# Performance work log

Hardware: AMD Instinct MI355X
Metric: run time of the kernel (lower is better)

Reference implementation:

```python
import jax, jax.numpy as jnp
import numpy as np


def _get_pairs(top_k_centers):
    """Returns (p0, p1) int32 arrays of shape [B, S]: for each object a, the
    IoU-best partner a', ordered so the larger-L1 box comes first (as in source)."""
    cx, cy, h, w = jnp.split(top_k_centers, 4, axis=-1)  # [B,S,1] each, cxcyhw
    box = jnp.concatenate([cx - 0.5 * w, cy - 0.5 * h, cx + 0.5 * w, cy + 0.5 * h], axis=-1)  # [B,S,4] xyxy
    S = box.shape[1]
    b1 = box[:, :, None, :]  # [B,S,1,4]
    b2 = box[:, None, :, :]  # [B,1,S,4]
    inter_mins = jnp.maximum(b1[..., :2], b2[..., :2])
    inter_maxs = jnp.maximum(b1[..., 2:], b2[..., 2:])  # NOTE: source uses maximum here (kept faithful)
    inter_wh = jnp.clip(inter_maxs - inter_mins, 0.0)
    inter_area = inter_wh[..., 0] * inter_wh[..., 1]  # [B,S,S]
    area = (box[..., 2] - box[..., 0]) * (box[..., 3] - box[..., 1])  # [B,S]
    union = area[:, :, None] + area[:, None, :] - inter_area
    iou = inter_area / union - jnp.eye(S, dtype=inter_area.dtype)
    partner = jnp.argmax(iou, axis=-1)  # [B,S] int
    self_idx = jnp.broadcast_to(jnp.arange(S), partner.shape)
    l1 = jnp.abs(box[..., 2] - box[..., 0]) + jnp.abs(box[..., 3] - box[..., 1])  # [B,S]
    l1_partner = jnp.take_along_axis(l1, partner, axis=-1)
    keep = l1 >= l1_partner  # larger-L1 element goes first
    p0 = jnp.where(keep, self_idx, partner)
    p1 = jnp.where(keep, partner, self_idx)
    return p0, p1


def _gather_pair(a2, p):
    # a2: [B,H,S,S]; p: [B,S]. out[b,h,a,c] = a2[b,h,p[b,a],p[b,c]]
    rows = jnp.take_along_axis(a2, p[:, None, :, None], axis=2)
    return jnp.take_along_axis(rows, p[:, None, None, :], axis=3)


def setup_inputs() -> dict:
    key = jax.random.key(0)
    kq, kk, kv, kc = jax.random.split(key, 4)
    B, H, S, D = 8, 8, 1024, 64
    return {
        "query": jax.random.normal(kq, (B, H, S, D), dtype=jnp.float32),
        "key": jax.random.normal(kk, (B, H, S, D), dtype=jnp.float32),
        "value": jax.random.normal(kv, (B, H, S, D), dtype=jnp.float32),
        "top_k_centers": jax.random.uniform(kc, (B, S, 4), dtype=jnp.float32),
    }


def reference(query, key, value, top_k_centers):
    B, H, S, D = query.shape
    p0, p1 = _get_pairs(top_k_centers)
    # A2(a,b) = <q_{pi_a}, k_{pi_b}> + <q_{pi_a'}, k_{pi_b'}>
    a2 = jnp.einsum('bhqd,bhkd->bhqk', query, key)  # [B,H,S,S]
    scores = (_gather_pair(a2, p0) + _gather_pair(a2, p1)) * (1.0 / np.sqrt(2.0 * D))
    attn = jax.nn.softmax(scores, axis=-1)
    o2 = jnp.einsum('bhqk,bhkd->bhqd', attn, value)  # [B,H,S,D]
    return o2.transpose(0, 2, 1, 3).reshape(B, S, H * D)
```

## Files before the change

### kernel.cpp

```cpp
#include <hip/hip_runtime.h>
#include <hip/hip_bf16.h>

#define B_ 8
#define H_ 8
#define S_ 1024
#define D_ 64
#define KT 32
#define NSTEP 16

typedef float f32x16 __attribute__((ext_vector_type(16)));
typedef short s16x8 __attribute__((ext_vector_type(8)));
typedef unsigned int u32;

#define CSCALE ((float)(1.4426950408889634 / 11.313708498984761))

static __device__ __forceinline__ unsigned short f2bf(float f) {
    union { float f; unsigned u; } v; v.f = f;
    unsigned r = v.u + 0x7FFF + ((v.u >> 16) & 1);
    return (unsigned short)(r >> 16);
}

static __device__ __forceinline__ u32 cvtpk(float lo, float hi) {
    u32 r;
    asm("v_cvt_pk_bf16_f32 %0, %1, %2" : "=v"(r) : "v"(lo), "v"(hi));
    return r;
}

static __device__ __forceinline__ void glds16(const void* g, void* l) {
    __builtin_amdgcn_global_load_lds(
        (const __attribute__((address_space(1))) unsigned int*)(uintptr_t)g,
        (__attribute__((address_space(3))) unsigned int*)(unsigned)(uintptr_t)l,
        16, 0, 0);
}

__global__ __launch_bounds__(256) void pairs_kernel(const float* __restrict__ centers,
                                                    const float* __restrict__ v,
                                                    int* __restrict__ p0,
                                                    int* __restrict__ p1,
                                                    unsigned short* __restrict__ Vt) {
#pragma clang fp contract(off)
    __shared__ __align__(16) float4 box4[S_];
    __shared__ float areas[S_], l1s[S_];
    __shared__ float tile[64][65];
    const int b = blockIdx.y;
    const int t = threadIdx.x;
    for (int idx = t; idx < S_; idx += 256) {
        const float4 c = *reinterpret_cast<const float4*>(centers + ((size_t)b * S_ + idx) * 4);
        const float cx = c.x, cy = c.y, hh = c.z, ww = c.w;
        const float x0 = cx - 0.5f * ww;
        const float y0 = cy - 0.5f * hh;
        const float x1 = cx + 0.5f * ww;
        const float y1 = cy + 0.5f * hh;
        box4[idx] = float4{x0, y0, x1, y1};
        areas[idx] = (x1 - x0) * (y1 - y0);
        l1s[idx] = fabsf(x1 - x0) + fabsf(y1 - y0);
    }
    __syncthreads();
    {
        const int i = blockIdx.x * 8 + (t >> 5);
        const int c32 = t & 31;
        const float4 bi = box4[i];
        const float ai = areas[i];
        float best = -1e38f; int arg = 0;
        #pragma unroll 4
        for (int it = 0; it < 32; ++it) {
            const int j = it * 32 + c32;
            const float4 bj = box4[j];
            const float aj = areas[j];
            float wx = fmaxf(bi.z, bj.z) - fmaxf(bi.x, bj.x);
            float wy = fmaxf(bi.w, bj.w) - fmaxf(bi.y, bj.y);
            wx = fmaxf(wx, 0.0f);
            wy = fmaxf(wy, 0.0f);
            const float inter = wx * wy;
            const float uni = (ai + aj) - inter;
            float val = inter / uni;
            if (j == i) val = val - 1.0f;
            if (val > best) { best = val; arg = j; }
        }
        #pragma unroll
        for (int m = 1; m <= 16; m <<= 1) {
            const float ob = __shfl_xor(best, m);
            const int oa = __shfl_xor(arg, m);
            if (ob > best || (ob == best && oa < arg)) { best = ob; arg = oa; }
        }
        if (c32 == 0) {
            const int partner = arg;
            const float l1i = l1s[i], l1p = l1s[partner];
            const int keep = (l1i >= l1p) ? 1 : 0;
            p0[b * S_ + i] = keep ? i : partner;
            p1[b * S_ + i] = keep ? partner : i;
        }
    }
    {
        const int unit = b * 128 + blockIdx.x;
        const int bh = unit >> 4;
        const int stile = unit & 15;
        const int s0 = stile * 64;
        const int kt0 = stile * 2;
        const float* vp = v + ((size_t)bh * S_ + s0) * D_;
        const int row = t >> 2, cpart = (t & 3) * 16;
        for (int jj = 0; jj < 4; ++jj) {
            const float4 x = *reinterpret_cast<const float4*>(&vp[(size_t)row * D_ + cpart + jj * 4]);
            tile[row][cpart + jj * 4 + 0] = x.x;
            tile[row][cpart + jj * 4 + 1] = x.y;
            tile[row][cpart + jj * 4 + 2] = x.z;
            tile[row][cpart + jj * 4 + 3] = x.w;
        }
        __syncthreads();
        unsigned short* VtB = Vt + (size_t)bh * 65536;
        for (int it = 0; it < 2; ++it) {
            const int flat = it * 256 + t;
            const int ktl = flat >> 8;
            const int L = (flat >> 6) & 3;
            const int lane = flat & 63;
            const int dt = L >> 1, ks = L & 1;
            const int d = dt * 32 + (lane & 31);
            const int sr = ktl * 32 + ks * 16 + ((lane >> 5) << 3);
            unsigned short hh[8];
            #pragma unroll
            for (int e = 0; e < 8; ++e) hh[e] = f2bf(tile[sr + e][d]);
            *reinterpret_cast<s16x8*>(VtB + ((size_t)((kt0 + ktl) * 4 + L) * 64 + lane) * 8) =
                *reinterpret_cast<s16x8*>(hh);
        }
    }
}

__global__ __launch_bounds__(256) void prep_k(const float* __restrict__ k,
                                              const int* __restrict__ p0,
                                              const int* __restrict__ p1,
                                              unsigned short* __restrict__ Kg) {
    const int gid = blockIdx.x;
    const int grp = (gid >> 3) & 15;
    const int bh = ((gid >> 7) << 3) | (gid & 7);
    const int b = bh >> 3;
    const int s0 = grp * 64;
    const int kt0 = grp * 2;
    const int t = threadIdx.x;
    const float* kp = k + (size_t)bh * S_ * D_;
    const int* p0b = p0 + b * S_;
    const int* p1b = p1 + b * S_;
    unsigned short* KgB = Kg + (size_t)bh * 131072;
    for (int it = 0; it < 4; ++it) {
        const int flat = it * 256 + t;
        const int ktl = flat >> 9;
        const int L = (flat >> 6) & 7;
        const int lane = flat & 63;
        const int s = s0 + ktl * 32 + (lane & 31);
        const int c = (L << 1) + (lane >> 5);
        const int i0 = p0b[s], i1 = p1b[s];
        const float* src = (c < 8) ? (kp + (size_t)i0 * D_ + c * 8)
                                   : (kp + (size_t)i1 * D_ + (c - 8) * 8);
        const float4 f0 = *reinterpret_cast<const float4*>(src);
        const float4 f1 = *reinterpret_cast<const float4*>(src + 4);
        union { u32 u[4]; s16x8 v; } pk;
        pk.u[0] = cvtpk(f0.x, f0.y);
        pk.u[1] = cvtpk(f0.z, f0.w);
        pk.u[2] = cvtpk(f1.x, f1.y);
        pk.u[3] = cvtpk(f1.z, f1.w);
        *reinterpret_cast<s16x8*>(KgB + ((size_t)((kt0 + ktl) * 8 + L) * 64 + lane) * 8) = pk.v;
    }
}

__global__ __launch_bounds__(256, 4) void attn_kernel(const float* __restrict__ q,
                                                      const unsigned short* __restrict__ Kg,
                                                      const unsigned short* __restrict__ Vt,
                                                      const int* __restrict__ p0,
                                                      const int* __restrict__ p1,
                                                      float* __restrict__ out) {
    __shared__ __align__(16) char smem[40960];
    auto Osh = reinterpret_cast<float(*)[32][66]>(smem);
    auto lsh = reinterpret_cast<float(*)[32]>(smem + 33792);

    const int tid = threadIdx.x;
    const int w = tid >> 6;
    const int r = w >> 1;
    const int s = w & 1;
    const int lane = tid & 63;
    const int qc = lane & 31;
    const int hi = lane >> 5;
    const int gid = blockIdx.x;
    const int rowtile = (gid >> 3) & 15;
    const int bh = ((gid >> 7) << 3) | (gid & 7);
    const int b = bh >> 3;
    const int h = bh & 7;

    const float* qp = q + (size_t)bh * S_ * D_;
    const unsigned short* KgB = Kg + (size_t)bh * 131072;
    const unsigned short* VtB = Vt + (size_t)bh * 65536;

    char* const strbase = smem + s * 20480;

    auto STAGE_K = [&](int t, int buf) {
        const int kt = s * NSTEP + t;
        char* base = strbase + buf * 8192;
        #pragma unroll
        for (int j = 0; j < 4; ++j) {
            const int L = r * 4 + j;
            glds16(KgB + ((size_t)(kt * 8 + L) * 64 + lane) * 8, base + L * 1024);
        }
    };
    auto STAGE_V = [&](int t) {
        const int kt = s * NSTEP + t;
        #pragma unroll
        for (int L = 0; L < 4; ++L)
            glds16(VtB + ((size_t)(kt * 4 + L) * 64 + lane) * 8, strbase + 16384 + L * 1024);
    };

    STAGE_K(0, 0);

    s16x8 qf[8];
    {
        const int qr = rowtile * 64 + r * 32 + qc;
        const int i0 = p0[b * S_ + qr], i1 = p1[b * S_ + qr];
        #pragma unroll
        for (int p = 0; p < 8; ++p) {
            const int k0 = 16 * p + 8 * hi;
            const float* src = (p < 4) ? (qp + (size_t)i0 * D_ + k0)
                                       : (qp + (size_t)i1 * D_ + (k0 - 64));
            const float4 f0 = *reinterpret_cast<const float4*>(src);
            const float4 f1 = *reinterpret_cast<const float4*>(src + 4);
            union { u32 u[4]; s16x8 v; } pk;
            pk.u[0] = cvtpk(f0.x * CSCALE, f0.y * CSCALE);
            pk.u[1] = cvtpk(f0.z * CSCALE, f0.w * CSCALE);
            pk.u[2] = cvtpk(f1.x * CSCALE, f1.y * CSCALE);
            pk.u[3] = cvtpk(f1.z * CSCALE, f1.w * CSCALE);
            qf[p] = pk.v;
        }
    }
    __syncthreads();

    f32x16 oacc0 = {}, oacc1 = {};
    f32x16 lsum = {};

    for (int t = 0; t < NSTEP; ++t) {
        const int buf = t & 1;
        STAGE_V(t);
        if (t + 1 < NSTEP) STAGE_K(t + 1, buf ^ 1);

        const unsigned short* KsT = reinterpret_cast<const unsigned short*>(strbase + buf * 8192);
        const unsigned short* VsT = reinterpret_cast<const unsigned short*>(strbase + 16384);

        f32x16 st = {};
        #pragma unroll
        for (int L = 0; L < 8; ++L) {
            const s16x8 kf = *reinterpret_cast<const s16x8*>(KsT + L * 512 + lane * 8);
            st = __builtin_amdgcn_mfma_f32_32x32x16_bf16(kf, qf[L], st, 0, 0, 0);
        }

        #pragma unroll
        for (int i = 0; i < 16; ++i) st[i] = exp2f(st[i]);
        lsum += st;

        u32 U[8];
        #pragma unroll
        for (int i = 0; i < 8; ++i) U[i] = cvtpk(st[2 * i], st[2 * i + 1]);

        if (t + 1 < NSTEP) asm volatile("s_waitcnt vmcnt(4)" ::: "memory");
        else               asm volatile("s_waitcnt vmcnt(0)" ::: "memory");
        __builtin_amdgcn_sched_barrier(0);

        #pragma unroll
        for (int ks = 0; ks < 2; ++ks) {
            const int a = 4 * ks;
            u32 w0 = U[a], w2 = U[a + 2];
            u32 w1 = U[a + 1], w3 = U[a + 3];
            asm("v_permlane32_swap_b32 %0, %1" : "+v"(w0), "+v"(w2));
            asm("v_permlane32_swap_b32 %0, %1" : "+v"(w1), "+v"(w3));
            union { u32 u[4]; s16x8 v; } pf;
            pf.u[0] = w0; pf.u[1] = w1; pf.u[2] = w2; pf.u[3] = w3;
            const s16x8 vf0 = *reinterpret_cast<const s16x8*>(VsT + ks * 512 + lane * 8);
            oacc0 = __builtin_amdgcn_mfma_f32_32x32x16_bf16(vf0, pf.v, oacc0, 0, 0, 0);
            const s16x8 vf1 = *reinterpret_cast<const s16x8*>(VsT + (2 + ks) * 512 + lane * 8);
            oacc1 = __builtin_amdgcn_mfma_f32_32x32x16_bf16(vf1, pf.v, oacc1, 0, 0, 0);
        }
        __syncthreads();
    }

    float l_run;
    {
        float a8[8];
        #pragma unroll
        for (int i = 0; i < 8; ++i) a8[i] = lsum[i] + lsum[i + 8];
        #pragma unroll
        for (int i = 0; i < 4; ++i) a8[i] += a8[i + 4];
        l_run = (a8[0] + a8[1]) + (a8[2] + a8[3]);
        l_run += __shfl_xor(l_run, 32);
    }

    #pragma unroll
    for (int i = 0; i < 16; ++i) {
        const int d0 = (i & 3) + 8 * (i >> 2) + 4 * hi;
        Osh[w][qc][d0] = oacc0[i];
        Osh[w][qc][32 + d0] = oacc1[i];
    }
    if (hi == 0) lsh[w][qc] = l_run;
    __syncthreads();

    const int row = tid >> 2;
    const int rr = row >> 5;
    const int lrow = row & 31;
    const int dc = (tid & 3) * 16;
    const int wa = rr * 2, wb = rr * 2 + 1;
    const float den = lsh[wa][lrow] + lsh[wb][lrow];
    const float inv = 1.0f / den;
    const int qrg = rowtile * 64 + row;
    float* orow = out + ((size_t)b * S_ + qrg) * (H_ * D_) + h * D_ + dc;
    #pragma unroll
    for (int e4 = 0; e4 < 4; ++e4) {
        float4 o;
        o.x = (Osh[wa][lrow][dc + e4 * 4 + 0] + Osh[wb][lrow][dc + e4 * 4 + 0]) * inv;
        o.y = (Osh[wa][lrow][dc + e4 * 4 + 1] + Osh[wb][lrow][dc + e4 * 4 + 1]) * inv;
        o.z = (Osh[wa][lrow][dc + e4 * 4 + 2] + Osh[wb][lrow][dc + e4 * 4 + 2]) * inv;
        o.w = (Osh[wa][lrow][dc + e4 * 4 + 3] + Osh[wb][lrow][dc + e4 * 4 + 3]) * inv;
        *reinterpret_cast<float4*>(orow + e4 * 4) = o;
    }
}

extern "C" void kernel_launch(void* const* d_in, const int* in_sizes, int n_in,
                              void* d_out, int out_size, void* d_ws, size_t ws_size,
                              hipStream_t stream) {
    (void)in_sizes; (void)n_in; (void)out_size; (void)ws_size;
    const float* q = (const float*)d_in[0];
    const float* k = (const float*)d_in[1];
    const float* v = (const float*)d_in[2];
    const float* c = (const float*)d_in[3];
    float* out = (float*)d_out;
    int* p0 = (int*)d_ws;
    int* p1 = p0 + B_ * S_;
    unsigned short* Kg = (unsigned short*)((char*)d_ws + 65536);
    unsigned short* Vt = Kg + (size_t)B_ * H_ * S_ * 128;
    pairs_kernel<<<dim3(128, 8), 256, 0, stream>>>(c, v, p0, p1, Vt);
    prep_k<<<dim3(1024), 256, 0, stream>>>(k, p0, p1, Kg);
    attn_kernel<<<dim3(1024), 256, 0, stream>>>(q, Kg, Vt, p0, p1, out);
}
```

Baseline: 70.74 us.

## Load V fragments directly into registers and unroll loop by two

V tiles were staged through LDS with global-to-LDS copies. They now go straight from global memory into registers, double-buffered across two register sets, and the main loop is unrolled by two so the buffer indices become constants. This frees the V region of shared memory, which lowers LDS use per block and may allow more blocks to be resident. It also drops the explicit vmcnt waits and the scheduling barrier, leaving the compiler to insert waits. The cost is higher VGPR pressure under the 256x4 launch bounds.

```diff
diff --git a/kernel.cpp b/kernel.cpp
--- a/kernel.cpp
+++ b/kernel.cpp
@@ -167,7 +167,7 @@
                                                       const int* __restrict__ p0,
                                                       const int* __restrict__ p1,
                                                       float* __restrict__ out) {
-    __shared__ __align__(16) char smem[40960];
+    __shared__ __align__(16) char smem[34304];
     auto Osh = reinterpret_cast<float(*)[32][66]>(smem);
     auto lsh = reinterpret_cast<float(*)[32]>(smem + 33792);
 
@@ -186,9 +186,9 @@
 
     const float* qp = q + (size_t)bh * S_ * D_;
     const unsigned short* KgB = Kg + (size_t)bh * 131072;
-    const unsigned short* VtB = Vt + (size_t)bh * 65536;
-
-    char* const strbase = smem + s * 20480;
+    const unsigned short* VtL = Vt + (size_t)bh * 65536 + (size_t)lane * 8;
+
+    char* const strbase = smem + s * 16384;
 
     auto STAGE_K = [&](int t, int buf) {
         const int kt = s * NSTEP + t;
@@ -199,13 +199,15 @@
             glds16(KgB + ((size_t)(kt * 8 + L) * 64 + lane) * 8, base + L * 1024);
         }
     };
-    auto STAGE_V = [&](int t) {
+    auto LOADV = [&](s16x8* vf, int t) {
         const int kt = s * NSTEP + t;
         #pragma unroll
         for (int L = 0; L < 4; ++L)
-            glds16(VtB + ((size_t)(kt * 4 + L) * 64 + lane) * 8, strbase + 16384 + L * 1024);
+            vf[L] = *reinterpret_cast<const s16x8*>(VtL + (size_t)(kt * 4 + L) * 512);
     };
 
+    s16x8 vfa[4], vfb[4];
+    LOADV(vfa, 0);
     STAGE_K(0, 0);
 
     s16x8 qf[8];
@@ -232,33 +234,20 @@
     f32x16 oacc0 = {}, oacc1 = {};
     f32x16 lsum = {};
 
-    for (int t = 0; t < NSTEP; ++t) {
-        const int buf = t & 1;
-        STAGE_V(t);
-        if (t + 1 < NSTEP) STAGE_K(t + 1, buf ^ 1);
-
+    auto COMPUTE = [&](int buf, const s16x8* vf) {
         const unsigned short* KsT = reinterpret_cast<const unsigned short*>(strbase + buf * 8192);
-        const unsigned short* VsT = reinterpret_cast<const unsigned short*>(strbase + 16384);
-
         f32x16 st = {};
         #pragma unroll
         for (int L = 0; L < 8; ++L) {
             const s16x8 kf = *reinterpret_cast<const s16x8*>(KsT + L * 512 + lane * 8);
             st = __builtin_amdgcn_mfma_f32_32x32x16_bf16(kf, qf[L], st, 0, 0, 0);
         }
-
         #pragma unroll
         for (int i = 0; i < 16; ++i) st[i] = exp2f(st[i]);
         lsum += st;
-
         u32 U[8];
         #pragma unroll
         for (int i = 0; i < 8; ++i) U[i] = cvtpk(st[2 * i], st[2 * i + 1]);
-
-        if (t + 1 < NSTEP) asm volatile("s_waitcnt vmcnt(4)" ::: "memory");
-        else               asm volatile("s_waitcnt vmcnt(0)" ::: "memory");
-        __builtin_amdgcn_sched_barrier(0);
-
         #pragma unroll
         for (int ks = 0; ks < 2; ++ks) {
             const int a = 4 * ks;
@@ -268,11 +257,21 @@
             asm("v_permlane32_swap_b32 %0, %1" : "+v"(w1), "+v"(w3));
             union { u32 u[4]; s16x8 v; } pf;
             pf.u[0] = w0; pf.u[1] = w1; pf.u[2] = w2; pf.u[3] = w3;
-            const s16x8 vf0 = *reinterpret_cast<const s16x8*>(VsT + ks * 512 + lane * 8);
-            oacc0 = __builtin_amdgcn_mfma_f32_32x32x16_bf16(vf0, pf.v, oacc0, 0, 0, 0);
-            const s16x8 vf1 = *reinterpret_cast<const s16x8*>(VsT + (2 + ks) * 512 + lane * 8);
-            oacc1 = __builtin_amdgcn_mfma_f32_32x32x16_bf16(vf1, pf.v, oacc1, 0, 0, 0);
-        }
+            oacc0 = __builtin_amdgcn_mfma_f32_32x32x16_bf16(vf[ks], pf.v, oacc0, 0, 0, 0);
+            oacc1 = __builtin_amdgcn_mfma_f32_32x32x16_bf16(vf[2 + ks], pf.v, oacc1, 0, 0, 0);
+        }
+    };
+
+    for (int t = 0; t < NSTEP; t += 2) {
+        LOADV(vfb, t + 1);
+        STAGE_K(t + 1, 1);
+        COMPUTE(0, vfa);
+        __syncthreads();
+        if (t + 2 < NSTEP) {
+            LOADV(vfa, t + 2);
+            STAGE_K(t + 2, 0);
+        }
+        COMPUTE(1, vfb);
         __syncthreads();
     }
 
```

Measured after the change: 121.0 us. 71.1% more time.
